# Optimization experiments

Hardware: AMD Instinct MI355X
Metric: run time of the kernel (lower is better)

Reference implementation:

```python
import jax, jax.numpy as jnp
import numpy as np

D = 4096  # domain size of every variable X, Y, Z, W


def setup_inputs() -> dict:
    key = jax.random.key(0)
    ks = jax.random.split(key, 7)
    theta0 = jax.random.normal(ks[0], (D, D), dtype=jnp.float32)  # clique (X, Y)
    theta1 = jax.random.normal(ks[1], (D, D), dtype=jnp.float32)  # clique (Y, Z)
    theta2 = jax.random.normal(ks[2], (D, D), dtype=jnp.float32)  # clique (Z, W)
    ops = {f"op{i}": jax.random.randint(ks[3 + i], (2, D), 0, D, dtype=jnp.int32)
           for i in range(4)}
    return {"theta0": theta0, "theta1": theta1, "theta2": theta2, **ops}


def _remap(proc, op, dom):
    # torch: zeros(dom).index_add_(0, op[1], proc[op[0]])
    return jnp.zeros((dom,), proc.dtype).at[op[1]].add(proc[op[0]])


def reference(theta0, theta1, theta2, op0, op1, op2, op3):
    dom = theta0.shape[0]
    # m0: clique0 -> clique1 (forward): sum over X (dim 0), remap Y, broadcast over Z
    m0 = _remap(jnp.sum(theta0, axis=0), op0, dom)
    theta1 = theta1 + m0[:, None]          # reshape_dims [True, False]
    # m1: clique1 -> clique2 (forward): sum over Y (dim 0), remap Z
    m1 = _remap(jnp.sum(theta1, axis=0), op1, dom)
    theta2 = theta2 + m1[:, None]
    # m2: clique2 -> clique1 (backward): sum over W (dim 1), subtract stored fwd msg m1
    m2 = _remap(jnp.sum(theta2, axis=1) - m1, op2, dom)
    theta1 = theta1 + m2[None, :]          # reshape_dims [False, True]
    # m3: clique1 -> clique0 (backward): sum over Z (dim 1), subtract stored fwd msg m0
    m3 = _remap(jnp.sum(theta1, axis=1) - m0, op3, dom)
    theta0 = theta0 + m3[None, :]
    return (theta0, theta1, theta2)
```

## Files before the change

kernel.cpp:

```cpp
#include <hip/hip_runtime.h>

#define D 4096


__global__ void colsum_kernel(const float* __restrict__ A, float* __restrict__ out) {
    const int ROWS = 64;
    int c4 = blockIdx.x * blockDim.x + threadIdx.x;
    int r0 = blockIdx.y * ROWS;
    const float4* A4 = (const float4*)A;
    float4 s = make_float4(0.f, 0.f, 0.f, 0.f);
    for (int r = 0; r < ROWS; ++r) {
        float4 v = A4[(size_t)(r0 + r) * (D / 4) + c4];
        s.x += v.x; s.y += v.y; s.z += v.z; s.w += v.w;
    }
    atomicAdd(&out[c4 * 4 + 0], s.x);
    atomicAdd(&out[c4 * 4 + 1], s.y);
    atomicAdd(&out[c4 * 4 + 2], s.z);
    atomicAdd(&out[c4 * 4 + 3], s.w);
}

__global__ void rowsum_kernel(const float* __restrict__ A, float* __restrict__ out) {
    int row = blockIdx.x;
    const float4* A4 = (const float4*)(A + (size_t)row * D);
    float s = 0.f;
    for (int i = threadIdx.x; i < D / 4; i += blockDim.x) {
        float4 v = A4[i];
        s += (v.x + v.y) + (v.z + v.w);
    }
    for (int o = 32; o > 0; o >>= 1) s += __shfl_down(s, o);
    __shared__ float red[4];
    int lane = threadIdx.x & 63, wid = threadIdx.x >> 6;
    if (lane == 0) red[wid] = s;
    __syncthreads();
    if (threadIdx.x == 0) out[row] = (red[0] + red[1]) + (red[2] + red[3]);
}


__device__ float block_sum_1024(float v, float* red) {
    for (int o = 32; o > 0; o >>= 1) v += __shfl_down(v, o);
    int lane = threadIdx.x & 63, wid = threadIdx.x >> 6;
    if (lane == 0) red[wid] = v;
    __syncthreads();
    if (threadIdx.x == 0) {
        float t = 0.f;
        for (int w = 0; w < 16; ++w) t += red[w];
        red[0] = t;
    }
    __syncthreads();
    return red[0];
}

__global__ void __launch_bounds__(1024) messages_kernel(
        const float* __restrict__ ws,
        const int* __restrict__ op0, const int* __restrict__ op1,
        const int* __restrict__ op2, const int* __restrict__ op3,
        float* __restrict__ ws_w) {
    const float* colsum0 = ws;
    const float* colsum1 = ws + D;
    const float* rowsum1 = ws + 2 * D;
    const float* rowsum2 = ws + 3 * D;
    float* g_m0 = ws_w + 4 * D;
    float* g_m1 = ws_w + 5 * D;
    float* g_m2 = ws_w + 6 * D;
    float* g_m3 = ws_w + 7 * D;

    __shared__ float m0[D], m1[D], m2[D];
    __shared__ float red[16];
    int tid = threadIdx.x;

    for (int i = tid; i < D; i += 1024) { m0[i] = 0.f; m1[i] = 0.f; m2[i] = 0.f; }
    __syncthreads();

    for (int i = tid; i < D; i += 1024)
        atomicAdd(&m0[op0[D + i]], colsum0[op0[i]]);
    __syncthreads();

    float p = 0.f;
    for (int i = tid; i < D; i += 1024) p += m0[i];
    float S0 = block_sum_1024(p, red);

    for (int i = tid; i < D; i += 1024)
        atomicAdd(&m1[op1[D + i]], colsum1[op1[i]] + S0);
    __syncthreads();

    for (int i = tid; i < D; i += 1024) {
        int src = op2[i];
        atomicAdd(&m2[op2[D + i]], rowsum2[src] + 4095.0f * m1[src]);
    }
    __syncthreads();

    p = 0.f;
    for (int i = tid; i < D; i += 1024) p += m2[i];
    float S2 = block_sum_1024(p, red);

    for (int i = tid; i < D; i += 1024) {
        int src = op3[i];
        atomicAdd(&g_m3[op3[D + i]], rowsum1[src] + 4095.0f * m0[src] + S2);
    }

    for (int i = tid; i < D; i += 1024) {
        g_m0[i] = m0[i]; g_m1[i] = m1[i]; g_m2[i] = m2[i];
    }
}


__global__ void apply_kernel(const float* __restrict__ t0, const float* __restrict__ t1,
                             const float* __restrict__ t2, const float* __restrict__ msgs,
                             float* __restrict__ out) {
    int b = blockIdx.x;
    int mat = b >> 12;
    int row = b & (D - 1);
    const float* m0 = msgs + 0 * D;
    const float* m1 = msgs + 1 * D;
    const float* m2 = msgs + 2 * D;
    const float* m3 = msgs + 3 * D;
    size_t base = (size_t)row * D;
    float4* dst = (float4*)(out + (size_t)mat * D * D + base);

    if (mat == 0) {
        const float4* src = (const float4*)(t0 + base);
        const float4* c4 = (const float4*)m3;
        for (int i = threadIdx.x; i < D / 4; i += blockDim.x) {
            float4 v = src[i], c = c4[i];
            dst[i] = make_float4(v.x + c.x, v.y + c.y, v.z + c.z, v.w + c.w);
        }
    } else if (mat == 1) {
        const float4* src = (const float4*)(t1 + base);
        const float4* c4 = (const float4*)m2;
        float r = m0[row];
        for (int i = threadIdx.x; i < D / 4; i += blockDim.x) {
            float4 v = src[i], c = c4[i];
            dst[i] = make_float4(v.x + r + c.x, v.y + r + c.y, v.z + r + c.z, v.w + r + c.w);
        }
    } else {
        const float4* src = (const float4*)(t2 + base);
        float r = m1[row];
        for (int i = threadIdx.x; i < D / 4; i += blockDim.x) {
            float4 v = src[i];
            dst[i] = make_float4(v.x + r, v.y + r, v.z + r, v.w + r);
        }
    }
}

extern "C" void kernel_launch(void* const* d_in, const int* in_sizes, int n_in,
                              void* d_out, int out_size, void* d_ws, size_t ws_size,
                              hipStream_t stream) {
    const float* t0 = (const float*)d_in[0];
    const float* t1 = (const float*)d_in[1];
    const float* t2 = (const float*)d_in[2];
    const int* op0 = (const int*)d_in[3];
    const int* op1 = (const int*)d_in[4];
    const int* op2 = (const int*)d_in[5];
    const int* op3 = (const int*)d_in[6];
    float* out = (float*)d_out;
    float* ws = (float*)d_ws;

    hipMemsetAsync(ws, 0, 2 * D * sizeof(float), stream);
    hipMemsetAsync(ws + 7 * D, 0, D * sizeof(float), stream);

    dim3 csGrid(D / 1024, D / 64);
    colsum_kernel<<<csGrid, 256, 0, stream>>>(t0, ws);
    colsum_kernel<<<csGrid, 256, 0, stream>>>(t1, ws + D);
    rowsum_kernel<<<D, 256, 0, stream>>>(t1, ws + 2 * D);
    rowsum_kernel<<<D, 256, 0, stream>>>(t2, ws + 3 * D);

    messages_kernel<<<1, 1024, 0, stream>>>(ws, op0, op1, op2, op3, ws);

    apply_kernel<<<3 * D, 256, 0, stream>>>(t0, t1, t2, ws + 4 * D, out);
}
```

Measured before the change: 161.8 us.

## Fuse reductions into one launch, prefetch indices in messages kernel, nontemporal apply stores

Merges the two column-sum and two row-sum kernels into a single launch, with rowsum now one wavefront per row. The messages kernel preloads all index and gather values into registers up front and accumulates m3 in shared memory instead of global atomics, which drops one memset. The apply kernel uses vector-type adds and nontemporal stores. This cuts launch overhead and serial latency in the single-block kernel, at the cost of more registers and shared memory.

```diff
diff --git a/kernel.cpp b/kernel.cpp
--- a/kernel.cpp
+++ b/kernel.cpp
@@ -2,52 +2,65 @@
 
 #define D 4096
 
-
-__global__ void colsum_kernel(const float* __restrict__ A, float* __restrict__ out) {
-    const int ROWS = 64;
-    int c4 = blockIdx.x * blockDim.x + threadIdx.x;
-    int r0 = blockIdx.y * ROWS;
-    const float4* A4 = (const float4*)A;
-    float4 s = make_float4(0.f, 0.f, 0.f, 0.f);
-    for (int r = 0; r < ROWS; ++r) {
-        float4 v = A4[(size_t)(r0 + r) * (D / 4) + c4];
-        s.x += v.x; s.y += v.y; s.z += v.z; s.w += v.w;
-    }
-    atomicAdd(&out[c4 * 4 + 0], s.x);
-    atomicAdd(&out[c4 * 4 + 1], s.y);
-    atomicAdd(&out[c4 * 4 + 2], s.z);
-    atomicAdd(&out[c4 * 4 + 3], s.w);
-}
-
-__global__ void rowsum_kernel(const float* __restrict__ A, float* __restrict__ out) {
-    int row = blockIdx.x;
-    const float4* A4 = (const float4*)(A + (size_t)row * D);
-    float s = 0.f;
-    for (int i = threadIdx.x; i < D / 4; i += blockDim.x) {
-        float4 v = A4[i];
-        s += (v.x + v.y) + (v.z + v.w);
-    }
-    for (int o = 32; o > 0; o >>= 1) s += __shfl_down(s, o);
-    __shared__ float red[4];
-    int lane = threadIdx.x & 63, wid = threadIdx.x >> 6;
-    if (lane == 0) red[wid] = s;
-    __syncthreads();
-    if (threadIdx.x == 0) out[row] = (red[0] + red[1]) + (red[2] + red[3]);
-}
-
-
-__device__ float block_sum_1024(float v, float* red) {
+typedef float fx4 __attribute__((ext_vector_type(4)));
+
+
+__global__ void __launch_bounds__(256) reduce_all_kernel(
+        const float* __restrict__ t0, const float* __restrict__ t1,
+        const float* __restrict__ t2, float* __restrict__ ws) {
+    int b = blockIdx.x;
+    if (b < 512) {
+        const float* A = (b < 256) ? t0 : t1;
+        float* out = ws + ((b < 256) ? 0 : D);
+        int lb = b & 255;
+        int c4 = (lb & 3) * 256 + threadIdx.x;
+        int r0 = (lb >> 2) * 64;
+        const fx4* A4 = (const fx4*)A;
+        fx4 s = (fx4){0.f, 0.f, 0.f, 0.f};
+        #pragma unroll 8
+        for (int r = 0; r < 64; ++r) {
+            s += A4[(size_t)(r0 + r) * (D / 4) + c4];
+        }
+        atomicAdd(&out[c4 * 4 + 0], s.x);
+        atomicAdd(&out[c4 * 4 + 1], s.y);
+        atomicAdd(&out[c4 * 4 + 2], s.z);
+        atomicAdd(&out[c4 * 4 + 3], s.w);
+    } else {
+        int lb = (b - 512) & 1023;
+        const float* A = (b < 1536) ? t1 : t2;
+        float* out = ws + ((b < 1536) ? 2 * D : 3 * D);
+        int wid = threadIdx.x >> 6, lane = threadIdx.x & 63;
+        int row = lb * 4 + wid;
+        const fx4* A4 = (const fx4*)(A + (size_t)row * D);
+        float s = 0.f;
+        #pragma unroll 4
+        for (int i = lane; i < D / 4; i += 64) {
+            fx4 v = A4[i];
+            s += (v.x + v.y) + (v.z + v.w);
+        }
+        #pragma unroll
+        for (int o = 32; o > 0; o >>= 1) s += __shfl_down(s, o);
+        if (lane == 0) out[row] = s;
+    }
+}
+
+
+__device__ __forceinline__ float block_sum_1024(float v, float* red) {
+    #pragma unroll
     for (int o = 32; o > 0; o >>= 1) v += __shfl_down(v, o);
     int lane = threadIdx.x & 63, wid = threadIdx.x >> 6;
     if (lane == 0) red[wid] = v;
     __syncthreads();
     if (threadIdx.x == 0) {
         float t = 0.f;
+        #pragma unroll
         for (int w = 0; w < 16; ++w) t += red[w];
         red[0] = t;
     }
     __syncthreads();
-    return red[0];
+    float r = red[0];
+    __syncthreads();
+    return r;
 }
 
 __global__ void __launch_bounds__(1024) messages_kernel(
@@ -59,54 +72,78 @@
     const float* colsum1 = ws + D;
     const float* rowsum1 = ws + 2 * D;
     const float* rowsum2 = ws + 3 * D;
-    float* g_m0 = ws_w + 4 * D;
-    float* g_m1 = ws_w + 5 * D;
-    float* g_m2 = ws_w + 6 * D;
-    float* g_m3 = ws_w + 7 * D;
-
-    __shared__ float m0[D], m1[D], m2[D];
+
+    __shared__ float m0[D], m1[D], m2[D], m3[D];
     __shared__ float red[16];
     int tid = threadIdx.x;
 
-    for (int i = tid; i < D; i += 1024) { m0[i] = 0.f; m1[i] = 0.f; m2[i] = 0.f; }
-    __syncthreads();
-
-    for (int i = tid; i < D; i += 1024)
-        atomicAdd(&m0[op0[D + i]], colsum0[op0[i]]);
+    int s0[4], d0[4], s1[4], d1[4], s2[4], d2[4], s3[4], d3[4];
+    #pragma unroll
+    for (int k = 0; k < 4; ++k) {
+        int i = tid + k * 1024;
+        s0[k] = op0[i]; d0[k] = op0[D + i];
+        s1[k] = op1[i]; d1[k] = op1[D + i];
+        s2[k] = op2[i]; d2[k] = op2[D + i];
+        s3[k] = op3[i]; d3[k] = op3[D + i];
+    }
+    float g0[4], g1[4], g2[4], g3[4];
+    #pragma unroll
+    for (int k = 0; k < 4; ++k) {
+        g0[k] = colsum0[s0[k]];
+        g1[k] = colsum1[s1[k]];
+        g2[k] = rowsum2[s2[k]];
+        g3[k] = rowsum1[s3[k]];
+    }
+
+    #pragma unroll
+    for (int k = 0; k < 4; ++k) {
+        int i = tid + k * 1024;
+        m0[i] = 0.f; m1[i] = 0.f; m2[i] = 0.f; m3[i] = 0.f;
+    }
+    __syncthreads();
+
+    #pragma unroll
+    for (int k = 0; k < 4; ++k) atomicAdd(&m0[d0[k]], g0[k]);
     __syncthreads();
 
     float p = 0.f;
-    for (int i = tid; i < D; i += 1024) p += m0[i];
+    #pragma unroll
+    for (int k = 0; k < 4; ++k) p += m0[tid + k * 1024];
     float S0 = block_sum_1024(p, red);
 
-    for (int i = tid; i < D; i += 1024)
-        atomicAdd(&m1[op1[D + i]], colsum1[op1[i]] + S0);
-    __syncthreads();
-
-    for (int i = tid; i < D; i += 1024) {
-        int src = op2[i];
-        atomicAdd(&m2[op2[D + i]], rowsum2[src] + 4095.0f * m1[src]);
-    }
+    #pragma unroll
+    for (int k = 0; k < 4; ++k) atomicAdd(&m1[d1[k]], g1[k] + S0);
+    __syncthreads();
+
+    #pragma unroll
+    for (int k = 0; k < 4; ++k)
+        atomicAdd(&m2[d2[k]], g2[k] + 4095.0f * m1[s2[k]]);
     __syncthreads();
 
     p = 0.f;
-    for (int i = tid; i < D; i += 1024) p += m2[i];
+    #pragma unroll
+    for (int k = 0; k < 4; ++k) p += m2[tid + k * 1024];
     float S2 = block_sum_1024(p, red);
 
-    for (int i = tid; i < D; i += 1024) {
-        int src = op3[i];
-        atomicAdd(&g_m3[op3[D + i]], rowsum1[src] + 4095.0f * m0[src] + S2);
-    }
-
-    for (int i = tid; i < D; i += 1024) {
-        g_m0[i] = m0[i]; g_m1[i] = m1[i]; g_m2[i] = m2[i];
-    }
-}
-
-
-__global__ void apply_kernel(const float* __restrict__ t0, const float* __restrict__ t1,
-                             const float* __restrict__ t2, const float* __restrict__ msgs,
-                             float* __restrict__ out) {
+    #pragma unroll
+    for (int k = 0; k < 4; ++k)
+        atomicAdd(&m3[d3[k]], g3[k] + 4095.0f * m0[s3[k]] + S2);
+    __syncthreads();
+
+    #pragma unroll
+    for (int k = 0; k < 4; ++k) {
+        int i = tid + k * 1024;
+        ws_w[4 * D + i] = m0[i];
+        ws_w[5 * D + i] = m1[i];
+        ws_w[6 * D + i] = m2[i];
+        ws_w[7 * D + i] = m3[i];
+    }
+}
+
+__global__ void __launch_bounds__(256) apply_kernel(
+        const float* __restrict__ t0, const float* __restrict__ t1,
+        const float* __restrict__ t2, const float* __restrict__ msgs,
+        float* __restrict__ out) {
     int b = blockIdx.x;
     int mat = b >> 12;
     int row = b & (D - 1);
@@ -115,29 +152,29 @@
     const float* m2 = msgs + 2 * D;
     const float* m3 = msgs + 3 * D;
     size_t base = (size_t)row * D;
-    float4* dst = (float4*)(out + (size_t)mat * D * D + base);
+    fx4* dst = (fx4*)(out + (size_t)mat * D * D + base);
 
     if (mat == 0) {
-        const float4* src = (const float4*)(t0 + base);
-        const float4* c4 = (const float4*)m3;
-        for (int i = threadIdx.x; i < D / 4; i += blockDim.x) {
-            float4 v = src[i], c = c4[i];
-            dst[i] = make_float4(v.x + c.x, v.y + c.y, v.z + c.z, v.w + c.w);
+        const fx4* src = (const fx4*)(t0 + base);
+        const fx4* c4 = (const fx4*)m3;
+        for (int i = threadIdx.x; i < D / 4; i += 256) {
+            fx4 r = src[i] + c4[i];
+            __builtin_nontemporal_store(r, &dst[i]);
         }
     } else if (mat == 1) {
-        const float4* src = (const float4*)(t1 + base);
-        const float4* c4 = (const float4*)m2;
-        float r = m0[row];
-        for (int i = threadIdx.x; i < D / 4; i += blockDim.x) {
-            float4 v = src[i], c = c4[i];
-            dst[i] = make_float4(v.x + r + c.x, v.y + r + c.y, v.z + r + c.z, v.w + r + c.w);
+        const fx4* src = (const fx4*)(t1 + base);
+        const fx4* c4 = (const fx4*)m2;
+        float rr = m0[row];
+        for (int i = threadIdx.x; i < D / 4; i += 256) {
+            fx4 r = src[i] + c4[i] + rr;
+            __builtin_nontemporal_store(r, &dst[i]);
         }
     } else {
-        const float4* src = (const float4*)(t2 + base);
-        float r = m1[row];
-        for (int i = threadIdx.x; i < D / 4; i += blockDim.x) {
-            float4 v = src[i];
-            dst[i] = make_float4(v.x + r, v.y + r, v.z + r, v.w + r);
+        const fx4* src = (const fx4*)(t2 + base);
+        float rr = m1[row];
+        for (int i = threadIdx.x; i < D / 4; i += 256) {
+            fx4 r = src[i] + rr;
+            __builtin_nontemporal_store(r, &dst[i]);
         }
     }
 }
@@ -156,15 +193,8 @@
     float* ws = (float*)d_ws;
 
     hipMemsetAsync(ws, 0, 2 * D * sizeof(float), stream);
-    hipMemsetAsync(ws + 7 * D, 0, D * sizeof(float), stream);
-
-    dim3 csGrid(D / 1024, D / 64);
-    colsum_kernel<<<csGrid, 256, 0, stream>>>(t0, ws);
-    colsum_kernel<<<csGrid, 256, 0, stream>>>(t1, ws + D);
-    rowsum_kernel<<<D, 256, 0, stream>>>(t1, ws + 2 * D);
-    rowsum_kernel<<<D, 256, 0, stream>>>(t2, ws + 3 * D);
-
+
+    reduce_all_kernel<<<2560, 256, 0, stream>>>(t0, t1, t2, ws);
     messages_kernel<<<1, 1024, 0, stream>>>(ws, op0, op1, op2, op3, ws);
-
     apply_kernel<<<3 * D, 256, 0, stream>>>(t0, t1, t2, ws + 4 * D, out);
 }
```

After: 143.8 us. -11.1%, faster.
